# Kernel optimization log

Measured on AMD Instinct MI355X. Metric: run time of the kernel, lower is better.

## Reference

```python
import jax, jax.numpy as jnp
import numpy as np

VOCAB = 50000
EMB = 128
ENC = 128
B = 256
K = 4            # tree arity
DEPTH = 5        # root at depth 0
N_NODES = (K ** (DEPTH + 1) - 1) // (K - 1)  # 1365, BFS order: children of i are K*i+1..K*i+K


def setup_inputs() -> dict:
    key = jax.random.key(0)
    ks = jax.random.split(key, 9)
    s = 0.05
    return {
        "tokens": jax.random.randint(ks[0], (N_NODES, B), 0, VOCAB, dtype=jnp.int32),
        "emb_table": jax.random.normal(ks[1], (VOCAB, EMB), jnp.float32) * s,
        "W_ih": jax.random.normal(ks[2], (3 * ENC, EMB), jnp.float32) * s,
        "W_hh": jax.random.normal(ks[3], (3 * ENC, ENC), jnp.float32) * s,
        "b_ih": jax.random.normal(ks[4], (3 * ENC,), jnp.float32) * s,
        "b_hh": jax.random.normal(ks[5], (3 * ENC,), jnp.float32) * s,
        "sent_weight": jax.random.normal(ks[6], (ENC, ENC), jnp.float32) * s,
        "sent_bias": jax.random.normal(ks[7], (1, ENC), jnp.float32) * s,
        "context_weight": jax.random.normal(ks[8], (ENC, 1), jnp.float32) * s,
    }


def _gru_step(x, h, W_ih, W_hh, b_ih, b_hh):
    # torch.nn.GRU single step: gates ordered (r, z, n)
    gi = x @ W_ih.T + b_ih
    gh = h @ W_hh.T + b_hh
    i_r, i_z, i_n = jnp.split(gi, 3, axis=-1)
    h_r, h_z, h_n = jnp.split(gh, 3, axis=-1)
    r = jax.nn.sigmoid(i_r + h_r)
    z = jax.nn.sigmoid(i_z + h_z)
    n = jnp.tanh(i_n + r * h_n)
    return (1.0 - z) * n + z * h


def _encode(tokens, emb_table, W_ih, W_hh, b_ih, b_hh, sent_weight, sent_bias, context_weight):
    # bottom-up over levels of a full K-ary tree; vectorized over (nodes-in-level, batch)
    level_starts = [(K ** d - 1) // (K - 1) for d in range(DEPTH + 2)]
    bsz = tokens.shape[1]
    outs = []
    child_h = None  # [n_{d+1}, B, ENC] hiddens of the level below, level-local order
    for d in range(DEPTH, -1, -1):
        s, e = level_starts[d], level_starts[d + 1]
        n_d = e - s
        x = emb_table[tokens[s:e]]  # [n_d, B, EMB]
        if child_h is None:
            h0 = jnp.zeros((n_d, bsz, ENC), x.dtype)  # leaves: no children
        else:
            # children of local node j are rows j*K..j*K+K-1 of child_h
            ch = child_h.reshape(n_d, K, bsz, ENC).transpose(1, 0, 2, 3)  # [K, n_d, B, E]
            u = jnp.tanh(jnp.einsum('knbe,ef->knbf', ch, sent_weight) + sent_bias)
            scores = jnp.tanh(jnp.einsum('knbe,eo->knbo', u, context_weight))[..., 0]  # [K, n_d, B]
            alpha = jax.nn.softmax(scores, axis=0)  # softmax over children, per (node, batch)
            h0 = jnp.einsum('knbe,knb->nbe', ch, alpha)
        hn = _gru_step(x, h0, W_ih, W_hh, b_ih, b_hh)  # [n_d, B, E]
        outs.append(hn)
        child_h = hn
    all_h = jnp.concatenate(outs, axis=0)  # [N_NODES, B, E]
    return jnp.max(all_h, axis=0)  # torch.max(node_list, 0)[0]


def reference(tokens, emb_table, W_ih, W_hh, b_ih, b_hh, sent_weight, sent_bias, context_weight):
    return _encode(tokens, emb_table, W_ih, W_hh, b_ih, b_hh,
                   sent_weight, sent_bias, context_weight)
```

## Files before the change

### kernel.cpp

```cpp
#include <hip/hip_runtime.h>
#include <hip/hip_bf16.h>
#include <math.h>

typedef short s8 __attribute__((ext_vector_type(8)));
typedef float f4 __attribute__((ext_vector_type(4)));
typedef unsigned short ushort_t;

__device__ __forceinline__ float fexp2f(float x) { return __builtin_amdgcn_exp2f(x); }
__device__ __forceinline__ float frcpf(float x)  { return __builtin_amdgcn_rcpf(x); }
__device__ __forceinline__ float sigf(float x) {
    return frcpf(1.f + fexp2f(x * -1.44269504f));
}
__device__ __forceinline__ float tanh_f(float x) {
    float e = fexp2f(x * 2.88539008f);
    return 1.f - 2.f * frcpf(e + 1.f);
}
__device__ __forceinline__ unsigned pk2(float a, float b) {
    __hip_bfloat162 r = __float22bfloat162_rn(make_float2(a, b));
    return *(unsigned*)&r;
}
__device__ __forceinline__ float b2f(ushort_t b) {
    return __uint_as_float(((unsigned)b) << 16);
}
__device__ __forceinline__ ushort_t f2b(float f) {
    unsigned u = __float_as_uint(f);
    u = (u + 0x7FFF + ((u >> 16) & 1)) >> 16;
    return (ushort_t)u;
}

#define EMB_N   6400000
#define W_N     49152
#define SW_N    16384
#define CVT_N   (EMB_N + 2 * W_N + SW_N)

__global__ __launch_bounds__(256) void cvt_kernel(
    const float* __restrict__ emb, const float* __restrict__ wih,
    const float* __restrict__ whh, const float* __restrict__ sw,
    ushort_t* __restrict__ embb, ushort_t* __restrict__ wihb,
    ushort_t* __restrict__ whhb, ushort_t* __restrict__ swtb)
{
    int i = (blockIdx.x * 256 + threadIdx.x) * 4;
    if (i >= CVT_N) return;
    if (i < EMB_N) {
        float4 v = *(const float4*)(emb + i);
        uint2 o; o.x = pk2(v.x, v.y); o.y = pk2(v.z, v.w);
        *(uint2*)(embb + i) = o;
    } else if (i < EMB_N + W_N) {
        int j = i - EMB_N;
        float4 v = *(const float4*)(wih + j);
        uint2 o; o.x = pk2(v.x, v.y); o.y = pk2(v.z, v.w);
        *(uint2*)(wihb + j) = o;
    } else if (i < EMB_N + 2 * W_N) {
        int j = i - EMB_N - W_N;
        float4 v = *(const float4*)(whh + j);
        uint2 o; o.x = pk2(v.x, v.y); o.y = pk2(v.z, v.w);
        *(uint2*)(whhb + j) = o;
    } else {
        int j = i - EMB_N - 2 * W_N;
        int f = j >> 7, e0 = j & 127;
        uint2 o;
        o.x = pk2(sw[(e0 + 0) * 128 + f], sw[(e0 + 1) * 128 + f]);
        o.y = pk2(sw[(e0 + 2) * 128 + f], sw[(e0 + 3) * 128 + f]);
        *(uint2*)(swtb + j) = o;
    }
}

__global__ __launch_bounds__(512, 2) void leafgru_mfma(
    const ushort_t* __restrict__ embb, const ushort_t* __restrict__ wihb,
    const float* __restrict__ bih, const float* __restrict__ bhh,
    ushort_t* __restrict__ hleaf)
{
    __shared__ ushort_t xs[128 * 136];

    const int t = threadIdx.x;
    const int base = blockIdx.x * 128;

    {
        int lr = t >> 2, c0 = (t & 3) * 32;
        const ushort_t* src = embb + (size_t)(base + lr) * 128 + c0;
        ushort_t* dst = &xs[lr * 136 + c0];
        #pragma unroll
        for (int i = 0; i < 4; ++i) *(s8*)(dst + 8 * i) = *(const s8*)(src + 8 * i);
    }

    const int lane = t & 63, w = t >> 6;
    const int quad = lane >> 4, l15 = lane & 15;
    const int gA = w * 16 + l15;
    const int g0 = w * 16 + quad * 4;

    s8 bwi[3][4];
    #pragma unroll
    for (int gm = 0; gm < 3; ++gm) {
        const ushort_t* wp = wihb + (size_t)(gm * 128 + gA) * 128 + quad * 8;
        #pragma unroll
        for (int s = 0; s < 4; ++s) bwi[gm][s] = *(const s8*)(wp + 32 * s);
    }
    float bR[4], bZ[4], biN[4], bhN[4];
    {
        float4 a = *(const float4*)(bih + g0);
        float4 b = *(const float4*)(bhh + g0);
        bR[0] = a.x + b.x; bR[1] = a.y + b.y; bR[2] = a.z + b.z; bR[3] = a.w + b.w;
        float4 c = *(const float4*)(bih + 128 + g0);
        float4 d = *(const float4*)(bhh + 128 + g0);
        bZ[0] = c.x + d.x; bZ[1] = c.y + d.y; bZ[2] = c.z + d.z; bZ[3] = c.w + d.w;
        float4 e = *(const float4*)(bih + 256 + g0);
        float4 f = *(const float4*)(bhh + 256 + g0);
        biN[0] = e.x; biN[1] = e.y; biN[2] = e.z; biN[3] = e.w;
        bhN[0] = f.x; bhN[1] = f.y; bhN[2] = f.z; bhN[3] = f.w;
    }

    __syncthreads();

    #pragma unroll 1
    for (int mt = 0; mt < 8; ++mt) {
        const int row = mt * 16 + l15;
        s8 ax[4];
        const ushort_t* ap = &xs[row * 136 + quad * 8];
        #pragma unroll
        for (int s = 0; s < 4; ++s) ax[s] = *(const s8*)(ap + 32 * s);

        f4 accR = (f4)0.f, accZ = (f4)0.f, accN = (f4)0.f;
        #pragma unroll
        for (int s = 0; s < 4; ++s) {
            accR = __builtin_amdgcn_mfma_f32_16x16x32_bf16(bwi[0][s], ax[s], accR, 0, 0, 0);
            accZ = __builtin_amdgcn_mfma_f32_16x16x32_bf16(bwi[1][s], ax[s], accZ, 0, 0, 0);
            accN = __builtin_amdgcn_mfma_f32_16x16x32_bf16(bwi[2][s], ax[s], accN, 0, 0, 0);
        }
        float hv[4];
        #pragma unroll
        for (int r = 0; r < 4; ++r) {
            float G = fexp2f((accR[r] + bR[r]) * -1.44269504f);
            float rr = frcpf(1.f + G);
            float an = accN[r] + biN[r] + rr * bhN[r];
            float E = fexp2f(an * 2.88539008f);
            float F = fexp2f((accZ[r] + bZ[r]) * -1.44269504f);
            float d = frcpf((E + 1.f) * (1.f + F));
            hv[r] = (E - 1.f) * F * d;
        }
        uint2 ov; ov.x = pk2(hv[0], hv[1]); ov.y = pk2(hv[2], hv[3]);
        *(uint2*)(hleaf + (size_t)(base + row) * 128 + g0) = ov;
    }
}

__global__ __launch_bounds__(512, 2) void leafattn_mfma(
    const int* __restrict__ tokens, const ushort_t* __restrict__ hleaf,
    const ushort_t* __restrict__ swt, const float* __restrict__ sb,
    const float* __restrict__ cw,
    ushort_t* __restrict__ h0out, ushort_t* __restrict__ pmaxs)
{
    __shared__ ushort_t xs[128 * 136];
    __shared__ float scp[8][128];
    __shared__ float sc[128];
    __shared__ float al[4][32];

    const int t = threadIdx.x;
    const int pn = blockIdx.x >> 3;
    const int b0 = (blockIdx.x & 7) * 32;

    {
        int lr = t >> 2, c0 = (t & 3) * 32;
        int node = 4 * pn + (lr >> 5), b = b0 + (lr & 31);
        int tok = tokens[(341 + node) * 256 + b];
        const ushort_t* src = hleaf + (size_t)tok * 128 + c0;
        ushort_t* dst = &xs[lr * 136 + c0];
        #pragma unroll
        for (int i = 0; i < 4; ++i) *(s8*)(dst + 8 * i) = *(const s8*)(src + 8 * i);
    }

    const int lane = t & 63, w = t >> 6;
    const int quad = lane >> 4, l15 = lane & 15;
    const int gA = w * 16 + l15;
    const int g0 = w * 16 + quad * 4;

    s8 bsw[4];
    {
        const ushort_t* wp = swt + (size_t)gA * 128 + quad * 8;
        #pragma unroll
        for (int s = 0; s < 4; ++s) bsw[s] = *(const s8*)(wp + 32 * s);
    }
    float sb4[4], cw4[4];
    {
        float4 a = *(const float4*)(sb + g0);
        float4 b = *(const float4*)(cw + g0);
        sb4[0] = a.x; sb4[1] = a.y; sb4[2] = a.z; sb4[3] = a.w;
        cw4[0] = b.x; cw4[1] = b.y; cw4[2] = b.z; cw4[3] = b.w;
    }
    __syncthreads();

    #pragma unroll 1
    for (int mt = 0; mt < 8; ++mt) {
        const int crow = mt * 16 + l15;
        s8 a[4];
        const ushort_t* ap = &xs[crow * 136 + quad * 8];
        #pragma unroll
        for (int s = 0; s < 4; ++s) a[s] = *(const s8*)(ap + 32 * s);

        f4 acc = (f4)0.f;
        #pragma unroll
        for (int s = 0; s < 4; ++s)
            acc = __builtin_amdgcn_mfma_f32_16x16x32_bf16(bsw[s], a[s], acc, 0, 0, 0);

        float part = 0.f;
        #pragma unroll
        for (int r = 0; r < 4; ++r)
            part += tanh_f(acc[r] + sb4[r]) * cw4[r];
        part += __shfl_xor(part, 16);
        part += __shfl_xor(part, 32);
        if (quad == 0) scp[w][crow] = part;
    }
    __syncthreads();

    if (t < 128) {
        float s = 0.f;
        #pragma unroll
        for (int ww = 0; ww < 8; ++ww) s += scp[ww][t];
        sc[t] = tanh_f(s);
    }
    __syncthreads();

    if (t < 32) {
        float s0 = sc[t], s1 = sc[32 + t], s2 = sc[64 + t], s3 = sc[96 + t];
        float m = fmaxf(fmaxf(s0, s1), fmaxf(s2, s3));
        float e0 = fexp2f((s0 - m) * 1.44269504f), e1 = fexp2f((s1 - m) * 1.44269504f);
        float e2 = fexp2f((s2 - m) * 1.44269504f), e3 = fexp2f((s3 - m) * 1.44269504f);
        float inv = frcpf(e0 + e1 + e2 + e3);
        al[0][t] = e0 * inv; al[1][t] = e1 * inv; al[2][t] = e2 * inv; al[3][t] = e3 * inv;
    }
    __syncthreads();

    {
        int bl = t >> 4, e0 = (t & 15) * 8;
        float a0 = al[0][bl], a1 = al[1][bl], a2 = al[2][bl], a3 = al[3][bl];
        s8 c0v = *(const s8*)&xs[(0 * 32 + bl) * 136 + e0];
        s8 c1v = *(const s8*)&xs[(1 * 32 + bl) * 136 + e0];
        s8 c2v = *(const s8*)&xs[(2 * 32 + bl) * 136 + e0];
        s8 c3v = *(const s8*)&xs[(3 * 32 + bl) * 136 + e0];
        float o[8], m[8];
        #pragma unroll
        for (int j = 0; j < 8; ++j) {
            float x0 = b2f((ushort_t)c0v[j]), x1 = b2f((ushort_t)c1v[j]);
            float x2 = b2f((ushort_t)c2v[j]), x3 = b2f((ushort_t)c3v[j]);
            o[j] = a0 * x0 + a1 * x1 + a2 * x2 + a3 * x3;
            m[j] = fmaxf(fmaxf(x0, x1), fmaxf(x2, x3));
        }
        uint4 ovv, mvv;
        ovv.x = pk2(o[0], o[1]); ovv.y = pk2(o[2], o[3]);
        ovv.z = pk2(o[4], o[5]); ovv.w = pk2(o[6], o[7]);
        mvv.x = pk2(m[0], m[1]); mvv.y = pk2(m[2], m[3]);
        mvv.z = pk2(m[4], m[5]); mvv.w = pk2(m[6], m[7]);
        size_t rh = ((size_t)pn * 256 + b0 + bl) * 128 + e0;
        *(uint4*)(h0out + rh) = ovv;
        size_t rp = ((size_t)(b0 + bl) * 320 + pn) * 128 + e0;
        *(uint4*)(pmaxs + rp) = mvv;
    }
}

__global__ __launch_bounds__(512, 2) void gru_mfma(
    const int* __restrict__ tokens, const ushort_t* __restrict__ embb,
    const ushort_t* __restrict__ wihb, const ushort_t* __restrict__ whhb,
    const float* __restrict__ bih, const float* __restrict__ bhh,
    const ushort_t* __restrict__ h0buf, ushort_t* __restrict__ hbuf,
    int lvl_start)
{
    __shared__ ushort_t xs[128 * 136];
    __shared__ ushort_t hs[128 * 136];

    const int t = threadIdx.x;
    const int base = blockIdx.x * 128;

    {
        int rl = t >> 2, c0 = (t & 3) * 32;
        int row = base + rl;
        int tok = tokens[(lvl_start + (row >> 8)) * 256 + (row & 255)];
        const ushort_t* src = embb + (size_t)tok * 128 + c0;
        ushort_t* dst = &xs[rl * 136 + c0];
        #pragma unroll
        for (int i = 0; i < 4; ++i) *(s8*)(dst + 8 * i) = *(const s8*)(src + 8 * i);
        const ushort_t* hsrc = h0buf + (size_t)row * 128 + c0;
        ushort_t* hdst = &hs[rl * 136 + c0];
        #pragma unroll
        for (int i = 0; i < 4; ++i) *(s8*)(hdst + 8 * i) = *(const s8*)(hsrc + 8 * i);
    }

    const int lane = t & 63, w = t >> 6;
    const int quad = lane >> 4, l15 = lane & 15;
    const int gA = w * 16 + l15;
    const int g0 = w * 16 + quad * 4;

    s8 bwi[3][4], bwh[3][4];
    #pragma unroll
    for (int gm = 0; gm < 3; ++gm) {
        const ushort_t* wp = wihb + (size_t)(gm * 128 + gA) * 128 + quad * 8;
        #pragma unroll
        for (int s = 0; s < 4; ++s) bwi[gm][s] = *(const s8*)(wp + 32 * s);
        const ushort_t* wp2 = whhb + (size_t)(gm * 128 + gA) * 128 + quad * 8;
        #pragma unroll
        for (int s = 0; s < 4; ++s) bwh[gm][s] = *(const s8*)(wp2 + 32 * s);
    }

    float bR[4], bZ[4], biN[4], bhN[4];
    {
        float4 a = *(const float4*)(bih + g0);
        float4 b = *(const float4*)(bhh + g0);
        bR[0] = a.x + b.x; bR[1] = a.y + b.y; bR[2] = a.z + b.z; bR[3] = a.w + b.w;
        float4 c = *(const float4*)(bih + 128 + g0);
        float4 d = *(const float4*)(bhh + 128 + g0);
        bZ[0] = c.x + d.x; bZ[1] = c.y + d.y; bZ[2] = c.z + d.z; bZ[3] = c.w + d.w;
        float4 e = *(const float4*)(bih + 256 + g0);
        float4 f = *(const float4*)(bhh + 256 + g0);
        biN[0] = e.x; biN[1] = e.y; biN[2] = e.z; biN[3] = e.w;
        bhN[0] = f.x; bhN[1] = f.y; bhN[2] = f.z; bhN[3] = f.w;
    }

    __syncthreads();

    #pragma unroll 1
    for (int mt = 0; mt < 8; ++mt) {
        const int row = mt * 16 + l15;
        s8 ax[4], ah[4];
        {
            const ushort_t* ap = &xs[row * 136 + quad * 8];
            #pragma unroll
            for (int s = 0; s < 4; ++s) ax[s] = *(const s8*)(ap + 32 * s);
            const ushort_t* hp = &hs[row * 136 + quad * 8];
            #pragma unroll
            for (int s = 0; s < 4; ++s) ah[s] = *(const s8*)(hp + 32 * s);
        }

        f4 accR = (f4)0.f, accZ = (f4)0.f, accN = (f4)0.f, accNh = (f4)0.f;
        #pragma unroll
        for (int s = 0; s < 4; ++s) {
            accR = __builtin_amdgcn_mfma_f32_16x16x32_bf16(bwi[0][s], ax[s], accR, 0, 0, 0);
            accZ = __builtin_amdgcn_mfma_f32_16x16x32_bf16(bwi[1][s], ax[s], accZ, 0, 0, 0);
            accN = __builtin_amdgcn_mfma_f32_16x16x32_bf16(bwi[2][s], ax[s], accN, 0, 0, 0);
        }
        #pragma unroll
        for (int s = 0; s < 4; ++s) {
            accR  = __builtin_amdgcn_mfma_f32_16x16x32_bf16(bwh[0][s], ah[s], accR, 0, 0, 0);
            accZ  = __builtin_amdgcn_mfma_f32_16x16x32_bf16(bwh[1][s], ah[s], accZ, 0, 0, 0);
            accNh = __builtin_amdgcn_mfma_f32_16x16x32_bf16(bwh[2][s], ah[s], accNh, 0, 0, 0);
        }

        float h0v[4];
        {
            short4 h04 = *(const short4*)&hs[row * 136 + g0];
            h0v[0] = b2f((ushort_t)h04.x); h0v[1] = b2f((ushort_t)h04.y);
            h0v[2] = b2f((ushort_t)h04.z); h0v[3] = b2f((ushort_t)h04.w);
        }
        float hv[4];
        #pragma unroll
        for (int r = 0; r < 4; ++r) {
            float G = fexp2f((accR[r] + bR[r]) * -1.44269504f);
            float rr = frcpf(1.f + G);
            float an = accN[r] + biN[r] + rr * (accNh[r] + bhN[r]);
            float E = fexp2f(an * 2.88539008f);
            float F = fexp2f((accZ[r] + bZ[r]) * -1.44269504f);
            float d = frcpf((E + 1.f) * (1.f + F));
            hv[r] = ((E - 1.f) * F + h0v[r] * (E + 1.f)) * d;
        }
        uint2 ov; ov.x = pk2(hv[0], hv[1]); ov.y = pk2(hv[2], hv[3]);
        *(uint2*)(hbuf + (size_t)(base + row) * 128 + g0) = ov;
    }
}

__global__ __launch_bounds__(512, 2) void attnmax_mfma(
    const ushort_t* __restrict__ hch, ushort_t* __restrict__ h0out,
    ushort_t* __restrict__ pmax,
    const ushort_t* __restrict__ swt, const float* __restrict__ sb,
    const float* __restrict__ cw)
{
    __shared__ ushort_t chs[128 * 136];
    __shared__ float scp[8][128];
    __shared__ float sc[128];
    __shared__ float al[4][32];

    const int t = threadIdx.x;
    const int pbase = blockIdx.x * 32;
    const int pnode = pbase >> 8;
    const int b0 = pbase & 255;

    {
        int lr = t >> 2, c0 = (t & 3) * 32;
        int k = lr >> 5, bl = lr & 31;
        const ushort_t* src = hch + ((size_t)(4 * pnode + k) * 256 + b0 + bl) * 128 + c0;
        ushort_t* dst = &chs[lr * 136 + c0];
        #pragma unroll
        for (int i = 0; i < 4; ++i) *(s8*)(dst + 8 * i) = *(const s8*)(src + 8 * i);
    }

    const int lane = t & 63, w = t >> 6;
    const int quad = lane >> 4, l15 = lane & 15;
    const int fA = w * 16 + l15;
    const int f0 = w * 16 + quad * 4;

    s8 bsw[4];
    {
        const ushort_t* wp = swt + (size_t)fA * 128 + quad * 8;
        #pragma unroll
        for (int s = 0; s < 4; ++s) bsw[s] = *(const s8*)(wp + 32 * s);
    }
    float sb4[4], cw4[4];
    {
        float4 a = *(const float4*)(sb + f0);
        float4 b = *(const float4*)(cw + f0);
        sb4[0] = a.x; sb4[1] = a.y; sb4[2] = a.z; sb4[3] = a.w;
        cw4[0] = b.x; cw4[1] = b.y; cw4[2] = b.z; cw4[3] = b.w;
    }
    __syncthreads();

    #pragma unroll 1
    for (int mt = 0; mt < 8; ++mt) {
        const int crow = mt * 16 + l15;
        s8 a[4];
        const ushort_t* ap = &chs[crow * 136 + quad * 8];
        #pragma unroll
        for (int s = 0; s < 4; ++s) a[s] = *(const s8*)(ap + 32 * s);

        f4 acc = (f4)0.f;
        #pragma unroll
        for (int s = 0; s < 4; ++s)
            acc = __builtin_amdgcn_mfma_f32_16x16x32_bf16(bsw[s], a[s], acc, 0, 0, 0);

        float part = 0.f;
        #pragma unroll
        for (int r = 0; r < 4; ++r)
            part += tanh_f(acc[r] + sb4[r]) * cw4[r];
        part += __shfl_xor(part, 16);
        part += __shfl_xor(part, 32);
        if (quad == 0) scp[w][crow] = part;
    }
    __syncthreads();

    if (t < 128) {
        float s = 0.f;
        #pragma unroll
        for (int ww = 0; ww < 8; ++ww) s += scp[ww][t];
        sc[t] = tanh_f(s);
    }
    __syncthreads();

    if (t < 32) {
        float s0 = sc[t], s1 = sc[32 + t], s2 = sc[64 + t], s3 = sc[96 + t];
        float m = fmaxf(fmaxf(s0, s1), fmaxf(s2, s3));
        float e0 = fexp2f((s0 - m) * 1.44269504f), e1 = fexp2f((s1 - m) * 1.44269504f);
        float e2 = fexp2f((s2 - m) * 1.44269504f), e3 = fexp2f((s3 - m) * 1.44269504f);
        float inv = frcpf(e0 + e1 + e2 + e3);
        al[0][t] = e0 * inv; al[1][t] = e1 * inv; al[2][t] = e2 * inv; al[3][t] = e3 * inv;
    }
    __syncthreads();

    {
        int bl = t >> 4, e0 = (t & 15) * 8;
        float a0 = al[0][bl], a1 = al[1][bl], a2 = al[2][bl], a3 = al[3][bl];
        s8 c0v = *(const s8*)&chs[(0 * 32 + bl) * 136 + e0];
        s8 c1v = *(const s8*)&chs[(1 * 32 + bl) * 136 + e0];
        s8 c2v = *(const s8*)&chs[(2 * 32 + bl) * 136 + e0];
        s8 c3v = *(const s8*)&chs[(3 * 32 + bl) * 136 + e0];
        float o[8], m[8];
        #pragma unroll
        for (int j = 0; j < 8; ++j) {
            float x0 = b2f((ushort_t)c0v[j]), x1 = b2f((ushort_t)c1v[j]);
            float x2 = b2f((ushort_t)c2v[j]), x3 = b2f((ushort_t)c3v[j]);
            o[j] = a0 * x0 + a1 * x1 + a2 * x2 + a3 * x3;
            m[j] = fmaxf(fmaxf(x0, x1), fmaxf(x2, x3));
        }
        uint4 ovv, mvv;
        ovv.x = pk2(o[0], o[1]); ovv.y = pk2(o[2], o[3]);
        ovv.z = pk2(o[4], o[5]); ovv.w = pk2(o[6], o[7]);
        mvv.x = pk2(m[0], m[1]); mvv.y = pk2(m[2], m[3]);
        mvv.z = pk2(m[4], m[5]); mvv.w = pk2(m[6], m[7]);
        size_t rh = ((size_t)pnode * 256 + b0 + bl) * 128 + e0;
        *(uint4*)(h0out + rh) = ovv;
        size_t rp = ((size_t)(b0 + bl) * 320 + 256 + pnode) * 128 + e0;
        *(uint4*)(pmax + rp) = mvv;
    }
}

__global__ __launch_bounds__(512, 1) void tail_kernel(
    const int* __restrict__ tokens, const ushort_t* __restrict__ embb,
    const ushort_t* __restrict__ wihb, const ushort_t* __restrict__ whhb,
    const float* __restrict__ bih, const float* __restrict__ bhh,
    const ushort_t* __restrict__ swt, const float* __restrict__ sb,
    const float* __restrict__ cw,
    const ushort_t* __restrict__ h0g,
    const ushort_t* __restrict__ pmax,
    float* __restrict__ out)
{
    __shared__ ushort_t xs[64 * 136];
    __shared__ ushort_t hnew[64 * 136];
    __shared__ ushort_t hs[64 * 136];
    __shared__ float scp[8][64];
    __shared__ float sc[64];
    __shared__ float al[4][16];
    __shared__ float smax[4][128];
    __shared__ float wpart[8][128];

    const int t = threadIdx.x;
    const int bb = blockIdx.x;
    const int lane = t & 63, w = t >> 6;
    const int quad = lane >> 4, l15 = lane & 15;
    const int gA = w * 16 + l15;
    const int g0 = w * 16 + quad * 4;

    s8 bwi[3][4], bwh[3][4];
    #pragma unroll
    for (int gm = 0; gm < 3; ++gm) {
        const ushort_t* wp = wihb + (size_t)(gm * 128 + gA) * 128 + quad * 8;
        #pragma unroll
        for (int s = 0; s < 4; ++s) bwi[gm][s] = *(const s8*)(wp + 32 * s);
        const ushort_t* wp2 = whhb + (size_t)(gm * 128 + gA) * 128 + quad * 8;
        #pragma unroll
        for (int s = 0; s < 4; ++s) bwh[gm][s] = *(const s8*)(wp2 + 32 * s);
    }
    float bR[4], bZ[4], biN[4], bhN[4];
    {
        float4 a = *(const float4*)(bih + g0);
        float4 b = *(const float4*)(bhh + g0);
        bR[0] = a.x + b.x; bR[1] = a.y + b.y; bR[2] = a.z + b.z; bR[3] = a.w + b.w;
        float4 c = *(const float4*)(bih + 128 + g0);
        float4 d = *(const float4*)(bhh + 128 + g0);
        bZ[0] = c.x + d.x; bZ[1] = c.y + d.y; bZ[2] = c.z + d.z; bZ[3] = c.w + d.w;
        float4 e = *(const float4*)(bih + 256 + g0);
        float4 f = *(const float4*)(bhh + 256 + g0);
        biN[0] = e.x; biN[1] = e.y; biN[2] = e.z; biN[3] = e.w;
        bhN[0] = f.x; bhN[1] = f.y; bhN[2] = f.z; bhN[3] = f.w;
    }
    s8 bsw[4];
    {
        const ushort_t* wp = swt + (size_t)gA * 128 + quad * 8;
        #pragma unroll
        for (int s = 0; s < 4; ++s) bsw[s] = *(const s8*)(wp + 32 * s);
    }
    float sb4[4], cw4[4];
    {
        float4 a = *(const float4*)(sb + g0);
        float4 b = *(const float4*)(cw + g0);
        sb4[0] = a.x; sb4[1] = a.y; sb4[2] = a.z; sb4[3] = a.w;
        cw4[0] = b.x; cw4[1] = b.y; cw4[2] = b.z; cw4[3] = b.w;
    }

    float vmax = -INFINITY;

    const int nodesA[4] = {64, 16, 4, 1};
    const int tok0A[4]  = {21, 5, 1, 0};

    #pragma unroll 1
    for (int L = 0; L < 4; ++L) {
        const int nodes = nodesA[L], tok0 = tok0A[L];
        const int R = (nodes < 16) ? 16 : nodes;
        const int mts = R >> 4;

        {
            int lr = t >> 3, c0 = (t & 7) * 16;
            if (lr < R) {
                int n = min(lr, nodes - 1);
                int tok = tokens[(tok0 + n) * 256 + bb];
                const ushort_t* src = embb + (size_t)tok * 128 + c0;
                ushort_t* dst = &xs[lr * 136 + c0];
                *(s8*)(dst)     = *(const s8*)(src);
                *(s8*)(dst + 8) = *(const s8*)(src + 8);
                if (L == 0) {
                    const ushort_t* hsrc = h0g + ((size_t)n * 256 + bb) * 128 + c0;
                    ushort_t* hdst = &hs[lr * 136 + c0];
                    *(s8*)(hdst)     = *(const s8*)(hsrc);
                    *(s8*)(hdst + 8) = *(const s8*)(hsrc + 8);
                }
            }
        }
        __syncthreads();

        for (int mt = 0; mt < mts; ++mt) {
            const int row = mt * 16 + l15;
            const int hr = min(row, nodes - 1);
            s8 ax[4], ah[4];
            {
                const ushort_t* ap = &xs[row * 136 + quad * 8];
                #pragma unroll
                for (int s = 0; s < 4; ++s) ax[s] = *(const s8*)(ap + 32 * s);
                const ushort_t* hp = &hs[hr * 136 + quad * 8];
                #pragma unroll
                for (int s = 0; s < 4; ++s) ah[s] = *(const s8*)(hp + 32 * s);
            }
            f4 accR = (f4)0.f, accZ = (f4)0.f, accN = (f4)0.f, accNh = (f4)0.f;
            #pragma unroll
            for (int s = 0; s < 4; ++s) {
                accR = __builtin_amdgcn_mfma_f32_16x16x32_bf16(bwi[0][s], ax[s], accR, 0, 0, 0);
                accZ = __builtin_amdgcn_mfma_f32_16x16x32_bf16(bwi[1][s], ax[s], accZ, 0, 0, 0);
                accN = __builtin_amdgcn_mfma_f32_16x16x32_bf16(bwi[2][s], ax[s], accN, 0, 0, 0);
            }
            #pragma unroll
            for (int s = 0; s < 4; ++s) {
                accR  = __builtin_amdgcn_mfma_f32_16x16x32_bf16(bwh[0][s], ah[s], accR, 0, 0, 0);
                accZ  = __builtin_amdgcn_mfma_f32_16x16x32_bf16(bwh[1][s], ah[s], accZ, 0, 0, 0);
                accNh = __builtin_amdgcn_mfma_f32_16x16x32_bf16(bwh[2][s], ah[s], accNh, 0, 0, 0);
            }
            float h0v[4];
            {
                short4 h04 = *(const short4*)&hs[hr * 136 + g0];
                h0v[0] = b2f((ushort_t)h04.x); h0v[1] = b2f((ushort_t)h04.y);
                h0v[2] = b2f((ushort_t)h04.z); h0v[3] = b2f((ushort_t)h04.w);
            }
            float hv[4];
            #pragma unroll
            for (int r = 0; r < 4; ++r) {
                float rr = sigf(accR[r] + bR[r]);
                float zz = sigf(accZ[r] + bZ[r]);
                float nn = tanh_f(accN[r] + biN[r] + rr * (accNh[r] + bhN[r]));
                hv[r] = nn + zz * (h0v[r] - nn);
            }
            uint2 ov; ov.x = pk2(hv[0], hv[1]); ov.y = pk2(hv[2], hv[3]);
            *(uint2*)&hnew[row * 136 + g0] = ov;
        }
        __syncthreads();

        {
            int col = t & 127, g = t >> 7;
            for (int r = g; r < R; r += 4)
                vmax = fmaxf(vmax, b2f(hnew[r * 136 + col]));
        }

        if (L < 3) {
            for (int mt = 0; mt < mts; ++mt) {
                const int crow = mt * 16 + l15;
                s8 a[4];
                const ushort_t* ap = &hnew[crow * 136 + quad * 8];
                #pragma unroll
                for (int s = 0; s < 4; ++s) a[s] = *(const s8*)(ap + 32 * s);
                f4 acc = (f4)0.f;
                #pragma unroll
                for (int s = 0; s < 4; ++s)
                    acc = __builtin_amdgcn_mfma_f32_16x16x32_bf16(bsw[s], a[s], acc, 0, 0, 0);
                float part = 0.f;
                #pragma unroll
                for (int r = 0; r < 4; ++r)
                    part += tanh_f(acc[r] + sb4[r]) * cw4[r];
                part += __shfl_xor(part, 16);
                part += __shfl_xor(part, 32);
                if (quad == 0) scp[w][crow] = part;
            }
            __syncthreads();
            if (t < R) {
                float s = 0.f;
                #pragma unroll
                for (int g = 0; g < 8; ++g) s += scp[g][t];
                sc[t] = tanh_f(s);
            }
            __syncthreads();
            const int P = nodes >> 2;
            if (t < P) {
                float s0 = sc[4 * t + 0], s1 = sc[4 * t + 1];
                float s2 = sc[4 * t + 2], s3 = sc[4 * t + 3];
                float m = fmaxf(fmaxf(s0, s1), fmaxf(s2, s3));
                float e0 = fexp2f((s0 - m) * 1.44269504f);
                float e1 = fexp2f((s1 - m) * 1.44269504f);
                float e2 = fexp2f((s2 - m) * 1.44269504f);
                float e3 = fexp2f((s3 - m) * 1.44269504f);
                float inv = frcpf(e0 + e1 + e2 + e3);
                al[0][t] = e0 * inv; al[1][t] = e1 * inv;
                al[2][t] = e2 * inv; al[3][t] = e3 * inv;
            }
            __syncthreads();
            if (t < 16 * P) {
                int bl = t >> 4, e0 = (t & 15) * 8;
                float a0 = al[0][bl], a1 = al[1][bl], a2 = al[2][bl], a3 = al[3][bl];
                s8 c0v = *(const s8*)&hnew[(4 * bl + 0) * 136 + e0];
                s8 c1v = *(const s8*)&hnew[(4 * bl + 1) * 136 + e0];
                s8 c2v = *(const s8*)&hnew[(4 * bl + 2) * 136 + e0];
                s8 c3v = *(const s8*)&hnew[(4 * bl + 3) * 136 + e0];
                float o[8];
                #pragma unroll
                for (int j = 0; j < 8; ++j) {
                    o[j] = a0 * b2f((ushort_t)c0v[j]) + a1 * b2f((ushort_t)c1v[j])
                         + a2 * b2f((ushort_t)c2v[j]) + a3 * b2f((ushort_t)c3v[j]);
                }
                uint4 ovv;
                ovv.x = pk2(o[0], o[1]); ovv.y = pk2(o[2], o[3]);
                ovv.z = pk2(o[4], o[5]); ovv.w = pk2(o[6], o[7]);
                *(uint4*)&hs[bl * 136 + e0] = ovv;
            }
            __syncthreads();
        }
    }

    smax[t >> 7][t & 127] = vmax;

    {
        int cg = t & 15;
        int ck = t >> 4;
        const ushort_t* base = pmax + (size_t)bb * 320 * 128 + cg * 8;
        float v8[8];
        #pragma unroll
        for (int j = 0; j < 8; ++j) v8[j] = -INFINITY;
        for (int s = ck; s < 320; s += 32) {
            s8 c = *(const s8*)(base + (size_t)s * 128);
            #pragma unroll
            for (int j = 0; j < 8; ++j) v8[j] = fmaxf(v8[j], b2f((ushort_t)c[j]));
        }
        #pragma unroll
        for (int j = 0; j < 8; ++j) {
            v8[j] = fmaxf(v8[j], __shfl_xor(v8[j], 16));
            v8[j] = fmaxf(v8[j], __shfl_xor(v8[j], 32));
        }
        if (lane < 16) {
            #pragma unroll
            for (int j = 0; j < 8; ++j) wpart[w][lane * 8 + j] = v8[j];
        }
    }
    __syncthreads();

    if (t < 128) {
        float m = wpart[0][t];
        #pragma unroll
        for (int ww = 1; ww < 8; ++ww) m = fmaxf(m, wpart[ww][t]);
        float own = fmaxf(fmaxf(smax[0][t], smax[1][t]),
                          fmaxf(smax[2][t], smax[3][t]));
        out[(size_t)bb * 128 + t] = fmaxf(m, own);
    }
}

extern "C" void kernel_launch(void* const* d_in, const int* in_sizes, int n_in,
                              void* d_out, int out_size, void* d_ws, size_t ws_size,
                              hipStream_t stream)
{
    const int*   tokens = (const int*)d_in[0];
    const float* emb    = (const float*)d_in[1];
    const float* Wih    = (const float*)d_in[2];
    const float* Whh    = (const float*)d_in[3];
    const float* bih    = (const float*)d_in[4];
    const float* bhh    = (const float*)d_in[5];
    const float* SW     = (const float*)d_in[6];
    const float* sb     = (const float*)d_in[7];
    const float* cw     = (const float*)d_in[8];
    float* out = (float*)d_out;

    ushort_t* embb = (ushort_t*)d_ws;
    ushort_t* wihb = embb + (size_t)EMB_N;
    ushort_t* whhb = wihb + W_N;
    ushort_t* swtb = whhb + W_N;
    ushort_t* h4   = swtb + SW_N;
    ushort_t* h0_4 = h4 + (size_t)256 * 32768;
    ushort_t* h0_3 = h0_4 + (size_t)256 * 32768;
    ushort_t* pmax = h0_3 + (size_t)64 * 32768;
    ushort_t* hleaf = h4;

    cvt_kernel<<<(CVT_N / 4 + 255) / 256, 256, 0, stream>>>(
        emb, Wih, Whh, SW, embb, wihb, whhb, swtb);

    leafgru_mfma<<<392, 512, 0, stream>>>(embb, wihb, bih, bhh, hleaf);

    leafattn_mfma<<<2048, 512, 0, stream>>>(
        tokens, hleaf, swtb, sb, cw, h0_4, pmax);

    gru_mfma<<<512, 512, 0, stream>>>(
        tokens, embb, wihb, whhb, bih, bhh, h0_4, h4, 85);
    attnmax_mfma<<<512, 512, 0, stream>>>(h4, h0_3, pmax, swtb, sb, cw);

    tail_kernel<<<256, 512, 0, stream>>>(
        tokens, embb, wihb, whhb, bih, bhh, swtb, sb, cw,
        h0_3, pmax, out);
}
```

Before: 186.2 us.

## Fuse leaf attention score into leaf GRU and child pooling into level-4 GRU

Leaf hidden states are already precomputed per vocabulary token. This change also computes each token's leaf attention score inside the leaf GRU kernel and stores it in a per-token table. The separate leaf-attention kernel is removed. The level-4 GRU kernel now gathers the four children's scores and hidden states by token, computes the softmax-weighted h0 and the running max inline, and writes pmax directly. This drops one launch and the h0_4 intermediate round trip, and it shrinks the attention matmul work to the vocabulary-sized table instead of every leaf instance. In exchange the GRU kernel loads take more gather traffic and more registers.

```diff
diff --git a/kernel.cpp b/kernel.cpp
--- a/kernel.cpp
+++ b/kernel.cpp
@@ -21,11 +21,6 @@
 }
 __device__ __forceinline__ float b2f(ushort_t b) {
     return __uint_as_float(((unsigned)b) << 16);
-}
-__device__ __forceinline__ ushort_t f2b(float f) {
-    unsigned u = __float_as_uint(f);
-    u = (u + 0x7FFF + ((u >> 16) & 1)) >> 16;
-    return (ushort_t)u;
 }
 
 #define EMB_N   6400000
@@ -68,9 +63,13 @@
 __global__ __launch_bounds__(512, 2) void leafgru_mfma(
     const ushort_t* __restrict__ embb, const ushort_t* __restrict__ wihb,
     const float* __restrict__ bih, const float* __restrict__ bhh,
-    ushort_t* __restrict__ hleaf)
+    const ushort_t* __restrict__ swt, const float* __restrict__ sb,
+    const float* __restrict__ cw,
+    ushort_t* __restrict__ hleaf, float* __restrict__ sleaf)
 {
     __shared__ ushort_t xs[128 * 136];
+    __shared__ ushort_t hnew[128 * 136];
+    __shared__ float scp[8][128];
 
     const int t = threadIdx.x;
     const int base = blockIdx.x * 128;
@@ -138,39 +137,10 @@
             hv[r] = (E - 1.f) * F * d;
         }
         uint2 ov; ov.x = pk2(hv[0], hv[1]); ov.y = pk2(hv[2], hv[3]);
+        *(uint2*)&hnew[row * 136 + g0] = ov;
         *(uint2*)(hleaf + (size_t)(base + row) * 128 + g0) = ov;
     }
-}
-
-__global__ __launch_bounds__(512, 2) void leafattn_mfma(
-    const int* __restrict__ tokens, const ushort_t* __restrict__ hleaf,
-    const ushort_t* __restrict__ swt, const float* __restrict__ sb,
-    const float* __restrict__ cw,
-    ushort_t* __restrict__ h0out, ushort_t* __restrict__ pmaxs)
-{
-    __shared__ ushort_t xs[128 * 136];
-    __shared__ float scp[8][128];
-    __shared__ float sc[128];
-    __shared__ float al[4][32];
-
-    const int t = threadIdx.x;
-    const int pn = blockIdx.x >> 3;
-    const int b0 = (blockIdx.x & 7) * 32;
-
-    {
-        int lr = t >> 2, c0 = (t & 3) * 32;
-        int node = 4 * pn + (lr >> 5), b = b0 + (lr & 31);
-        int tok = tokens[(341 + node) * 256 + b];
-        const ushort_t* src = hleaf + (size_t)tok * 128 + c0;
-        ushort_t* dst = &xs[lr * 136 + c0];
-        #pragma unroll
-        for (int i = 0; i < 4; ++i) *(s8*)(dst + 8 * i) = *(const s8*)(src + 8 * i);
-    }
-
-    const int lane = t & 63, w = t >> 6;
-    const int quad = lane >> 4, l15 = lane & 15;
-    const int gA = w * 16 + l15;
-    const int g0 = w * 16 + quad * 4;
+    __syncthreads();
 
     s8 bsw[4];
     {
@@ -185,13 +155,12 @@
         sb4[0] = a.x; sb4[1] = a.y; sb4[2] = a.z; sb4[3] = a.w;
         cw4[0] = b.x; cw4[1] = b.y; cw4[2] = b.z; cw4[3] = b.w;
     }
-    __syncthreads();
 
     #pragma unroll 1
     for (int mt = 0; mt < 8; ++mt) {
         const int crow = mt * 16 + l15;
         s8 a[4];
-        const ushort_t* ap = &xs[crow * 136 + quad * 8];
+        const ushort_t* ap = &hnew[crow * 136 + quad * 8];
         #pragma unroll
         for (int s = 0; s < 4; ++s) a[s] = *(const s8*)(ap + 32 * s);
 
@@ -214,72 +183,72 @@
         float s = 0.f;
         #pragma unroll
         for (int ww = 0; ww < 8; ++ww) s += scp[ww][t];
-        sc[t] = tanh_f(s);
-    }
-    __syncthreads();
-
-    if (t < 32) {
-        float s0 = sc[t], s1 = sc[32 + t], s2 = sc[64 + t], s3 = sc[96 + t];
+        sleaf[base + t] = tanh_f(s);
+    }
+}
+
+__global__ __launch_bounds__(512, 2) void gru_fused(
+    const int* __restrict__ tokens, const ushort_t* __restrict__ embb,
+    const ushort_t* __restrict__ hleaf, const float* __restrict__ sleaf,
+    const ushort_t* __restrict__ wihb, const ushort_t* __restrict__ whhb,
+    const float* __restrict__ bih, const float* __restrict__ bhh,
+    ushort_t* __restrict__ hbuf, ushort_t* __restrict__ pmaxs)
+{
+    __shared__ ushort_t xs[128 * 136];
+    __shared__ ushort_t hs[128 * 136];
+
+    const int t = threadIdx.x;
+    const int base = blockIdx.x * 128;
+
+    {
+        int rl = t >> 2, c0 = (t & 3) * 32;
+        int row = base + rl;
+        int node = row >> 8, b = row & 255;
+        int tok = tokens[(85 + node) * 256 + b];
+        const ushort_t* src = embb + (size_t)tok * 128 + c0;
+        ushort_t* dst = &xs[rl * 136 + c0];
+        #pragma unroll
+        for (int i = 0; i < 4; ++i) *(s8*)(dst + 8 * i) = *(const s8*)(src + 8 * i);
+
+        int lt0 = tokens[(341 + 4 * node + 0) * 256 + b];
+        int lt1 = tokens[(341 + 4 * node + 1) * 256 + b];
+        int lt2 = tokens[(341 + 4 * node + 2) * 256 + b];
+        int lt3 = tokens[(341 + 4 * node + 3) * 256 + b];
+        float s0 = sleaf[lt0], s1 = sleaf[lt1], s2 = sleaf[lt2], s3 = sleaf[lt3];
         float m = fmaxf(fmaxf(s0, s1), fmaxf(s2, s3));
         float e0 = fexp2f((s0 - m) * 1.44269504f), e1 = fexp2f((s1 - m) * 1.44269504f);
         float e2 = fexp2f((s2 - m) * 1.44269504f), e3 = fexp2f((s3 - m) * 1.44269504f);
         float inv = frcpf(e0 + e1 + e2 + e3);
-        al[0][t] = e0 * inv; al[1][t] = e1 * inv; al[2][t] = e2 * inv; al[3][t] = e3 * inv;
-    }
-    __syncthreads();
-
-    {
-        int bl = t >> 4, e0 = (t & 15) * 8;
-        float a0 = al[0][bl], a1 = al[1][bl], a2 = al[2][bl], a3 = al[3][bl];
-        s8 c0v = *(const s8*)&xs[(0 * 32 + bl) * 136 + e0];
-        s8 c1v = *(const s8*)&xs[(1 * 32 + bl) * 136 + e0];
-        s8 c2v = *(const s8*)&xs[(2 * 32 + bl) * 136 + e0];
-        s8 c3v = *(const s8*)&xs[(3 * 32 + bl) * 136 + e0];
-        float o[8], m[8];
-        #pragma unroll
-        for (int j = 0; j < 8; ++j) {
-            float x0 = b2f((ushort_t)c0v[j]), x1 = b2f((ushort_t)c1v[j]);
-            float x2 = b2f((ushort_t)c2v[j]), x3 = b2f((ushort_t)c3v[j]);
-            o[j] = a0 * x0 + a1 * x1 + a2 * x2 + a3 * x3;
-            m[j] = fmaxf(fmaxf(x0, x1), fmaxf(x2, x3));
-        }
-        uint4 ovv, mvv;
-        ovv.x = pk2(o[0], o[1]); ovv.y = pk2(o[2], o[3]);
-        ovv.z = pk2(o[4], o[5]); ovv.w = pk2(o[6], o[7]);
-        mvv.x = pk2(m[0], m[1]); mvv.y = pk2(m[2], m[3]);
-        mvv.z = pk2(m[4], m[5]); mvv.w = pk2(m[6], m[7]);
-        size_t rh = ((size_t)pn * 256 + b0 + bl) * 128 + e0;
-        *(uint4*)(h0out + rh) = ovv;
-        size_t rp = ((size_t)(b0 + bl) * 320 + pn) * 128 + e0;
-        *(uint4*)(pmaxs + rp) = mvv;
-    }
-}
-
-__global__ __launch_bounds__(512, 2) void gru_mfma(
-    const int* __restrict__ tokens, const ushort_t* __restrict__ embb,
-    const ushort_t* __restrict__ wihb, const ushort_t* __restrict__ whhb,
-    const float* __restrict__ bih, const float* __restrict__ bhh,
-    const ushort_t* __restrict__ h0buf, ushort_t* __restrict__ hbuf,
-    int lvl_start)
-{
-    __shared__ ushort_t xs[128 * 136];
-    __shared__ ushort_t hs[128 * 136];
-
-    const int t = threadIdx.x;
-    const int base = blockIdx.x * 128;
-
-    {
-        int rl = t >> 2, c0 = (t & 3) * 32;
-        int row = base + rl;
-        int tok = tokens[(lvl_start + (row >> 8)) * 256 + (row & 255)];
-        const ushort_t* src = embb + (size_t)tok * 128 + c0;
-        ushort_t* dst = &xs[rl * 136 + c0];
-        #pragma unroll
-        for (int i = 0; i < 4; ++i) *(s8*)(dst + 8 * i) = *(const s8*)(src + 8 * i);
-        const ushort_t* hsrc = h0buf + (size_t)row * 128 + c0;
+        float a0 = e0 * inv, a1 = e1 * inv, a2 = e2 * inv, a3 = e3 * inv;
+
+        const ushort_t* p0 = hleaf + (size_t)lt0 * 128 + c0;
+        const ushort_t* p1 = hleaf + (size_t)lt1 * 128 + c0;
+        const ushort_t* p2 = hleaf + (size_t)lt2 * 128 + c0;
+        const ushort_t* p3 = hleaf + (size_t)lt3 * 128 + c0;
         ushort_t* hdst = &hs[rl * 136 + c0];
-        #pragma unroll
-        for (int i = 0; i < 4; ++i) *(s8*)(hdst + 8 * i) = *(const s8*)(hsrc + 8 * i);
+        ushort_t* pmp = pmaxs + ((size_t)b * 320 + node) * 128 + c0;
+        #pragma unroll
+        for (int i = 0; i < 4; ++i) {
+            s8 v0 = *(const s8*)(p0 + 8 * i);
+            s8 v1 = *(const s8*)(p1 + 8 * i);
+            s8 v2 = *(const s8*)(p2 + 8 * i);
+            s8 v3 = *(const s8*)(p3 + 8 * i);
+            float o[8], mm[8];
+            #pragma unroll
+            for (int j = 0; j < 8; ++j) {
+                float x0 = b2f((ushort_t)v0[j]), x1 = b2f((ushort_t)v1[j]);
+                float x2 = b2f((ushort_t)v2[j]), x3 = b2f((ushort_t)v3[j]);
+                o[j]  = a0 * x0 + a1 * x1 + a2 * x2 + a3 * x3;
+                mm[j] = fmaxf(fmaxf(x0, x1), fmaxf(x2, x3));
+            }
+            uint4 ovv, mvv;
+            ovv.x = pk2(o[0], o[1]);  ovv.y = pk2(o[2], o[3]);
+            ovv.z = pk2(o[4], o[5]);  ovv.w = pk2(o[6], o[7]);
+            mvv.x = pk2(mm[0], mm[1]); mvv.y = pk2(mm[2], mm[3]);
+            mvv.z = pk2(mm[4], mm[5]); mvv.w = pk2(mm[6], mm[7]);
+            *(uint4*)(hdst + 8 * i) = ovv;
+            *(uint4*)(pmp + 8 * i)  = mvv;
+        }
     }
 
     const int lane = t & 63, w = t >> 6;
@@ -733,26 +702,25 @@
     const float* cw     = (const float*)d_in[8];
     float* out = (float*)d_out;
 
-    ushort_t* embb = (ushort_t*)d_ws;
-    ushort_t* wihb = embb + (size_t)EMB_N;
-    ushort_t* whhb = wihb + W_N;
-    ushort_t* swtb = whhb + W_N;
-    ushort_t* h4   = swtb + SW_N;
-    ushort_t* h0_4 = h4 + (size_t)256 * 32768;
-    ushort_t* h0_3 = h0_4 + (size_t)256 * 32768;
-    ushort_t* pmax = h0_3 + (size_t)64 * 32768;
-    ushort_t* hleaf = h4;
+    ushort_t* embb  = (ushort_t*)d_ws;
+    ushort_t* wihb  = embb + (size_t)EMB_N;
+    ushort_t* whhb  = wihb + W_N;
+    ushort_t* swtb  = whhb + W_N;
+    ushort_t* hleaf = swtb + SW_N;
+    float*    sleaf = (float*)(hleaf + (size_t)50176 * 128);
+    ushort_t* h4    = (ushort_t*)(sleaf + 50176);
+    ushort_t* h0_3  = h4 + (size_t)256 * 32768;
+    ushort_t* pmax  = h0_3 + (size_t)64 * 32768;
 
     cvt_kernel<<<(CVT_N / 4 + 255) / 256, 256, 0, stream>>>(
         emb, Wih, Whh, SW, embb, wihb, whhb, swtb);
 
-    leafgru_mfma<<<392, 512, 0, stream>>>(embb, wihb, bih, bhh, hleaf);
-
-    leafattn_mfma<<<2048, 512, 0, stream>>>(
-        tokens, hleaf, swtb, sb, cw, h0_4, pmax);
-
-    gru_mfma<<<512, 512, 0, stream>>>(
-        tokens, embb, wihb, whhb, bih, bhh, h0_4, h4, 85);
+    leafgru_mfma<<<392, 512, 0, stream>>>(
+        embb, wihb, bih, bhh, swtb, sb, cw, hleaf, sleaf);
+
+    gru_fused<<<512, 512, 0, stream>>>(
+        tokens, embb, hleaf, sleaf, wihb, whhb, bih, bhh, h4, pmax);
+
     attnmax_mfma<<<512, 512, 0, stream>>>(h4, h0_3, pmax, swtb, sb, cw);
 
     tail_kernel<<<256, 512, 0, stream>>>(
```

Result: no change. 184.6 us (-0.9%).
